# Performance work log

Measured on AMD Instinct MI355X. Metric: run time of the kernel, lower is better.

## Reference

```python
import jax, jax.numpy as jnp
from jax import lax
import numpy as np

B, S_SRC, S_TRG = 128, 128, 64
LEX_V, LEX_D = 32000, 300
NT_V, NT_D = 128, 128
H, CTX, ATT = 1024, 300, 100
DIN = LEX_D + 2 * NT_D + CTX  # decoder LSTM input: [ans_embed | context]


def setup_inputs():
    key = jax.random.key(0)
    ks = iter(jax.random.split(key, 40))
    g = lambda shape, s=0.05: jax.random.normal(next(ks), shape, dtype=jnp.float32) * s
    src_seqs = jax.random.randint(next(ks), (B, S_SRC), 1, LEX_V)
    src_lengths = jnp.sort(jax.random.randint(next(ks), (B,), 1, S_SRC + 1))[::-1]
    src_lengths = src_lengths.at[0].set(S_SRC)  # packed seqs sorted desc, max len = S_SRC
    trg_nt = jax.random.randint(next(ks), (B, S_TRG), 1, NT_V)
    par_nt = jax.random.randint(next(ks), (B, S_TRG), 1, NT_V)
    par_lex = jax.random.randint(next(ks), (B, S_TRG), 1, LEX_V)
    lex_emb = g((LEX_V, LEX_D), 1.0).at[0].set(0.0)  # padding_idx=0 zeroed
    nt_emb = g((NT_V, NT_D), 1.0).at[0].set(0.0)
    return {
        'src_seqs': src_seqs, 'src_lengths': src_lengths,
        'trg_nt': trg_nt, 'par_nt': par_nt, 'par_lex': par_lex,
        'lex_emb': lex_emb, 'nt_emb': nt_emb,
        'enc_Wih': g((4 * H, LEX_D)), 'enc_Whh': g((4 * H, H)), 'enc_b': g((4 * H,)),
        'dec_Wih': g((4 * H, DIN)), 'dec_Whh': g((4 * H, H)), 'dec_b': g((4 * H,)),
        'Wh1': g((2 * H, H)), 'bh1': g((2 * H,)), 'Wh2': g((H, 2 * H)), 'bh2': g((H,)),
        'Wc1': g((2 * H, H)), 'bc1': g((2 * H,)), 'Wc2': g((H, 2 * H)), 'bc2': g((H,)),
        'Wa': g((ATT, H)), 'ba': g((ATT,)),
        'Wqk': g((ATT, H)), 'bqk': g((ATT,)),
        'Wqv': g((CTX, H)), 'bqv': g((CTX,)),
    }


def lstm_cell(x, h, c, Wih, Whh, b):
    z = x @ Wih.T + h @ Whh.T + b
    i, f, g, o = jnp.split(z, 4, axis=-1)  # torch gate order i,f,g,o
    c2 = jax.nn.sigmoid(f) * c + jax.nn.sigmoid(i) * jnp.tanh(g)
    h2 = jax.nn.sigmoid(o) * jnp.tanh(c2)
    return h2, c2


def reference(src_seqs, src_lengths, trg_nt, par_nt, par_lex,
              lex_emb, nt_emb,
              enc_Wih, enc_Whh, enc_b, dec_Wih, dec_Whh, dec_b,
              Wh1, bh1, Wh2, bh2, Wc1, bc1, Wc2, bc2,
              Wa, ba, Wqk, bqk, Wqv, bqv):
    # ---- encoder LSTM over packed src (mask past lengths) ----
    src_embed = lex_emb[src_seqs]                       # (B,S,LEX_D)
    h0 = jnp.zeros((B, H), jnp.float32)

    def enc_step(carry, inp):
        h, c = carry
        xt, t = inp
        h2, c2 = lstm_cell(xt, h, c, enc_Wih, enc_Whh, enc_b)
        valid = (t < src_lengths)[:, None]
        h = jnp.where(valid, h2, h)
        c = jnp.where(valid, c2, c)
        return (h, c), jnp.where(valid, h2, 0.0)

    (hT, cT), outs = lax.scan(enc_step, (h0, h0),
                              (jnp.swapaxes(src_embed, 0, 1), jnp.arange(S_SRC)))
    src_hidden = jnp.swapaxes(outs, 0, 1)               # (B,S,H), zeros past length

    # ---- init decoder hidden via MLP transforms ----
    dh = jax.nn.relu(hT @ Wh1.T + bh1) @ Wh2.T + bh2
    dc = jax.nn.relu(cT @ Wc1.T + bc1) @ Wc2.T + bc2

    # ---- attention keys/values (src-side is step-invariant) ----
    q_key = jnp.tanh(src_hidden @ Wqk.T + bqk)          # (B,S,ATT)
    q_value = src_hidden @ Wqv.T + bqv                  # (B,S,CTX)
    mask = jnp.arange(S_SRC)[None, :] < src_lengths[:, None]

    ans_embed = jnp.concatenate(
        [nt_emb[trg_nt], nt_emb[par_nt], lex_emb[par_lex]], axis=2)  # (B,T,LEX_D+2*NT_D)

    def dec_step(carry, xt):
        h, c = carry
        a_key = jnp.tanh(h @ Wa.T + ba)                 # (B,ATT)
        energy = jnp.einsum('bsk,bk->bs', q_key, a_key)
        energy = jnp.where(mask, energy, -1e9)
        w = jax.nn.softmax(energy, axis=1)
        context = jnp.einsum('bs,bsd->bd', w, q_value)  # (B,CTX)
        inp = jnp.concatenate([xt, context], axis=1)    # (B,DIN)
        h2, c2 = lstm_cell(inp, h, c, dec_Wih, dec_Whh, dec_b)
        return (h2, c2), h2

    _, dec_outs = lax.scan(dec_step, (dh, dc), jnp.swapaxes(ans_embed, 0, 1))
    return jnp.swapaxes(dec_outs, 0, 1)                 # (B,T,H)
```

## Files before the change

kernel.cpp:

```cpp
#include <hip/hip_runtime.h>


constexpr int B_ = 128, S_ = 128, T_ = 64, H_ = 1024;
constexpr int KE_ = 1344;
constexpr int KD_ = 1920;
constexpr int KCE = KE_ / 32, KCD = KD_ / 32;

using bf16x8 = __attribute__((ext_vector_type(8))) __bf16;
using f32x4  = __attribute__((ext_vector_type(4))) float;
using ull = unsigned long long;

union Pack8 { ull q[2]; bf16x8 v; };

__device__ __forceinline__ float ldf(const void* p, size_t i, bool bf) {
  return bf ? (float)((const __bf16*)p)[i] : ((const float*)p)[i];
}
__device__ __forceinline__ float sigf(float x) { return 1.f / (1.f + __expf(-x)); }
__device__ __forceinline__ float tanf_(float x) { return 1.f - 2.f / (1.f + __expf(2.f * x)); }

__device__ __forceinline__ ull al8(const ull* p) {
  return __hip_atomic_load(p, __ATOMIC_RELAXED, __HIP_MEMORY_SCOPE_AGENT);
}
__device__ __forceinline__ void as8(ull* p, ull v) {
  __hip_atomic_store(p, v, __ATOMIC_RELAXED, __HIP_MEMORY_SCOPE_AGENT);
}

__device__ __forceinline__ void gbar(unsigned* bar, int bb, unsigned ep) {
  __syncthreads();
  if (threadIdx.x == 0)
    __hip_atomic_fetch_add(&bar[(bb & 15) * 32], 1u, __ATOMIC_RELAXED,
                           __HIP_MEMORY_SCOPE_AGENT);
  if (threadIdx.x < 16) {
    const unsigned tgt = ep * 16;
    while (__hip_atomic_load(&bar[threadIdx.x * 32], __ATOMIC_RELAXED,
                             __HIP_MEMORY_SCOPE_AGENT) < tgt)
      __builtin_amdgcn_s_sleep(2);
  }
  __syncthreads();
}

__global__ void sniff(const void* __restrict__ lex, int* __restrict__ flag) {
  if (threadIdx.x == 0 && blockIdx.x == 0) {
    const unsigned short* u = (const unsigned short*)lex;
    int garbage = 0;
    for (int i = 0; i < 64; ++i) {
      unsigned short v = u[1000000 + 2 * i];
      int ex = (v >> 7) & 0xFF;
      bool sane = ((v & 0x7FFF) == 0) || (ex >= 107 && ex <= 147);
      if (!sane) ++garbage;
    }
    *flag = (garbage >= 16) ? 0 : 1;
  }
}

__global__ void cvt_to_f32(const void* __restrict__ src, float* __restrict__ dst,
                           int n, const int* __restrict__ flag) {
  int i = blockIdx.x * blockDim.x + threadIdx.x;
  bool bf = *flag != 0;
  if (i < n) dst[i] = ldf(src, i, bf);
}

__global__ void f2b(const float* __restrict__ s, __bf16* __restrict__ d, int n) {
  int i = blockIdx.x * blockDim.x + threadIdx.x;
  if (i < n) d[i] = (__bf16)s[i];
}

__global__ void zero_state(__bf16* __restrict__ h, float* __restrict__ c) {
  int i = blockIdx.x * blockDim.x + threadIdx.x;
  if (i < B_ * H_) { h[i] = (__bf16)0.f; c[i] = 0.f; }
}

__global__ void zero_bar(unsigned* __restrict__ bar) {
  bar[threadIdx.x] = 0u;
}

__global__ void build_w_enc_sw(const void* __restrict__ Wih, const void* __restrict__ Whh,
                               __bf16* __restrict__ W, const int* __restrict__ flag) {
  int bid = blockIdx.x;
  int ug = bid >> 1, nt = bid & 1;
  bool bf = *flag != 0;
  for (int i = threadIdx.x; i < KCE * 512; i += blockDim.x) {
    int kc = i >> 9, rem = i & 511, lane = rem >> 3, j = rem & 7;
    int col = lane & 15, quad = lane >> 4;
    int gate = nt * 2 + (col >> 3), ul = col & 7;
    int r = gate * 1024 + ug * 8 + ul;
    int k = kc * 32 + quad * 8 + j;
    float v;
    if (k < 320) v = (k < 300) ? ldf(Wih, (size_t)r * 300 + k, bf) : 0.f;
    else         v = ldf(Whh, (size_t)r * 1024 + (k - 320), bf);
    W[(((size_t)bid * KCE + kc) * 64 + lane) * 8 + j] = (__bf16)v;
  }
}

__global__ void build_w_dec_sw(const void* __restrict__ Wih, const void* __restrict__ Whh,
                               __bf16* __restrict__ W, const int* __restrict__ flag) {
  int bid = blockIdx.x;
  int ug = bid >> 1, nt = bid & 1;
  bool bf = *flag != 0;
  for (int i = threadIdx.x; i < KCD * 512; i += blockDim.x) {
    int kc = i >> 9, rem = i & 511, lane = rem >> 3, j = rem & 7;
    int col = lane & 15, quad = lane >> 4;
    int gate = nt * 2 + (col >> 3), ul = col & 7;
    int r = gate * 1024 + ug * 8 + ul;
    int k = kc * 32 + quad * 8 + j;
    float v;
    if (k < 576)      v = (k < 556) ? ldf(Wih, (size_t)r * 856 + k, bf) : 0.f;
    else if (k < 896) { int kk = k - 576; v = (kk < 300) ? ldf(Wih, (size_t)r * 856 + 556 + kk, bf) : 0.f; }
    else              v = ldf(Whh, (size_t)r * 1024 + (k - 896), bf);
    W[(((size_t)bid * KCD + kc) * 64 + lane) * 8 + j] = (__bf16)v;
  }
}

__global__ void pad_cvt(const void* __restrict__ src, __bf16* __restrict__ dst,
                        int N, int K, int Kpad, const int* __restrict__ flag) {
  int n = blockIdx.x;
  bool bf = *flag != 0;
  for (int k = threadIdx.x; k < Kpad; k += blockDim.x) {
    float v = (n < N && k < K) ? ldf(src, (size_t)n * K + k, bf) : 0.f;
    dst[(size_t)n * Kpad + k] = (__bf16)v;
  }
}

__global__ void gather_emb(const void* __restrict__ lex, const int* __restrict__ seq,
                           __bf16* __restrict__ dst, const int* __restrict__ flag) {
  int blk = blockIdx.x;
  int t = blk >> 7, b = blk & 127;
  int id = seq[b * S_ + t];
  bool bf = *flag != 0;
  for (int k = threadIdx.x; k < 320; k += blockDim.x) {
    float v = (k < 300) ? ldf(lex, (size_t)id * 300 + k, bf) : 0.f;
    dst[(size_t)blk * 320 + k] = (__bf16)v;
  }
}

__global__ void gather_ans(const void* __restrict__ nt, const void* __restrict__ lex,
                           const int* __restrict__ trg, const int* __restrict__ par,
                           const int* __restrict__ plex, __bf16* __restrict__ dst,
                           const int* __restrict__ flag) {
  int blk = blockIdx.x;
  int t = blk >> 7, b = blk & 127;
  int i1 = trg[b * T_ + t], i2 = par[b * T_ + t], i3 = plex[b * T_ + t];
  bool bf = *flag != 0;
  for (int k = threadIdx.x; k < 576; k += blockDim.x) {
    float v = 0.f;
    if (k < 128)      v = ldf(nt, (size_t)i1 * 128 + k, bf);
    else if (k < 256) v = ldf(nt, (size_t)i2 * 128 + (k - 128), bf);
    else if (k < 556) v = ldf(lex, (size_t)i3 * 300 + (k - 256), bf);
    dst[(size_t)blk * 576 + k] = (__bf16)v;
  }
}

template <int ACT, bool WB, bool WF>
__global__ __launch_bounds__(256)
void gemm16(const __bf16* __restrict__ A, int lda,
            const __bf16* __restrict__ W, int K,
            const float* __restrict__ bias, int Nreal,
            __bf16* __restrict__ Cb, float* __restrict__ Cf, int ldc) {
  const int lane = threadIdx.x & 63;
  const int wave = threadIdx.x >> 6;
  const int col = lane & 15, quad = lane >> 4, koff = quad * 8;
  const int n0 = blockIdx.x * 16;
  const int m0 = blockIdx.y * 64 + wave * 16;
  f32x4 acc = {0.f, 0.f, 0.f, 0.f};
  const __bf16* ap = A + (size_t)(m0 + col) * lda + koff;
  const __bf16* wp = W + (size_t)(n0 + col) * K + koff;
  for (int k0 = 0; k0 < K; k0 += 32) {
    bf16x8 af = *(const bf16x8*)(ap + k0);
    bf16x8 bf = *(const bf16x8*)(wp + k0);
    acc = __builtin_amdgcn_mfma_f32_16x16x32_bf16(af, bf, acc, 0, 0, 0);
  }
  int n = n0 + col;
  float bv = (n < Nreal) ? bias[n] : 0.f;
#pragma unroll
  for (int r = 0; r < 4; ++r) {
    int m = m0 + quad * 4 + r;
    float v = acc[r] + bv;
    if (ACT == 1) v = fmaxf(v, 0.f);
    if (ACT == 2) v = tanf_(v);
    size_t idx = (size_t)m * ldc + n;
    if (WB) Cb[idx] = (__bf16)v;
    if (WF) Cf[idx] = v;
  }
}

__global__ void transpose_qk(const float* __restrict__ q, float* __restrict__ qT) {
  int b = blockIdx.x;
  for (int i = threadIdx.x; i < 100 * 128; i += blockDim.x) {
    int k = i >> 7, s = i & 127;
    qT[((size_t)b * 100 + k) * 128 + s] = q[((size_t)b * 128 + s) * 112 + k];
  }
}

struct EncArgs {
  const __bf16* wE; const float* bEncF; const __bf16* embE;
  __bf16* h0; __bf16* h1; float* cE; const int* lens; __bf16* SH; unsigned* bar;
};

__global__ __launch_bounds__(256, 1)
void enc_coop(EncArgs a) {
  extern __shared__ char smem[];
  __bf16* Wl = (__bf16*)smem;
  float* zb = (float*)(smem + 2 * KCE * 512 * 2);
  __bf16* hbuf = (__bf16*)(smem + 2 * KCE * 512 * 2 + 64 * 33 * 4);
  const int bb = blockIdx.x;
  const int ug = bb >> 1, mh = bb & 1;
  {
    const uint4* src = (const uint4*)(a.wE + (size_t)ug * 2 * KCE * 512);
    uint4* dst = (uint4*)Wl;
    for (int i = threadIdx.x; i < 2 * KCE * 512 * 2 / 16; i += 256) dst[i] = src[i];
  }
  const int tid = threadIdx.x;
  const int lane = tid & 63, wave = tid >> 6;
  const int col = lane & 15, quad = lane >> 4, koff = quad * 8;
  const int am = mh * 64 + wave * 16 + col;
  __syncthreads();

  for (int t = 0; t < S_; ++t) {
    const __bf16* hR = (t & 1) ? a.h1 : a.h0;
    __bf16* hW = (t & 1) ? a.h0 : a.h1;
    f32x4 acc0 = {0.f, 0.f, 0.f, 0.f}, acc1 = {0.f, 0.f, 0.f, 0.f};
    const __bf16* embRow = a.embE + ((size_t)t * B_ + am) * 320 + koff;
    const ull* hRow8 = (const ull*)(hR + (size_t)am * H_) + quad * 2;
#pragma unroll
    for (int kc = 0; kc < KCE; ++kc) {
      const int k0 = kc * 32;
      bf16x8 af;
      if (k0 < 320) {
        af = *(const bf16x8*)(embRow + k0);
      } else {
        Pack8 u2;
        u2.q[0] = al8(hRow8 + ((k0 - 320) >> 2));
        u2.q[1] = al8(hRow8 + ((k0 - 320) >> 2) + 1);
        af = u2.v;
      }
      bf16x8 b0 = *(const bf16x8*)(Wl + ((size_t)(0 * KCE + kc) * 64 + lane) * 8);
      bf16x8 b1 = *(const bf16x8*)(Wl + ((size_t)(1 * KCE + kc) * 64 + lane) * 8);
      acc0 = __builtin_amdgcn_mfma_f32_16x16x32_bf16(af, b0, acc0, 0, 0, 0);
      acc1 = __builtin_amdgcn_mfma_f32_16x16x32_bf16(af, b1, acc1, 0, 0, 0);
    }
#pragma unroll
    for (int r = 0; r < 4; ++r) {
      int ml = wave * 16 + quad * 4 + r;
      zb[ml * 33 + col] = acc0[r];
      zb[ml * 33 + 16 + col] = acc1[r];
    }
    __syncthreads();
#pragma unroll
    for (int p = 0; p < 2; ++p) {
      int idx = tid + p * 256;
      int ml = idx >> 3, u = idx & 7;
      int m = mh * 64 + ml, j = ug * 8 + u;
      float ig = sigf(zb[ml * 33 + u]       + a.bEncF[j]);
      float fg = sigf(zb[ml * 33 + 8 + u]   + a.bEncF[1024 + j]);
      float gg = tanf_(zb[ml * 33 + 16 + u] + a.bEncF[2048 + j]);
      float og = sigf(zb[ml * 33 + 24 + u]  + a.bEncF[3072 + j]);
      size_t sidx = (size_t)m * H_ + j;
      float cOld = a.cE[sidx];
      float c2 = fg * cOld + ig * gg;
      float h2 = og * tanf_(c2);
      bool valid = t < a.lens[m];
      a.cE[sidx] = valid ? c2 : cOld;
      hbuf[ml * 8 + u] = (__bf16)h2;
      a.SH[((size_t)m * S_ + t) * H_ + j] = valid ? (__bf16)h2 : (__bf16)0.f;
    }
    __syncthreads();
    if (tid < 128) {
      int ml = tid >> 1, u0 = (tid & 1) * 4;
      int m = mh * 64 + ml;
      ull nv = *(const ull*)(hbuf + ml * 8 + u0);
      if (t >= a.lens[m]) nv = al8((const ull*)(hR + (size_t)m * H_ + ug * 8 + u0));
      as8((ull*)(hW + (size_t)m * H_ + ug * 8 + u0), nv);
    }
    if (t != S_ - 1) gbar(a.bar, bb, t + 1);
  }
}

struct DecArgs {
  const __bf16* wD; const float* bDecF; const __bf16* ansP;
  __bf16* h0; __bf16* h1; float* cD; const int* lens;
  const __bf16* waB; const float* baF; const float* qkT; const float* qval;
  __bf16* ctx; void* out; const int* flag; unsigned* bar;
};

__global__ __launch_bounds__(256, 1)
void dec_coop(DecArgs a) {
  extern __shared__ char smem[];
  __bf16* Wl = (__bf16*)smem;
  float* zb = (float*)(smem + 2 * KCD * 512 * 2);
  __bf16* hbuf = (__bf16*)(smem + 2 * KCD * 512 * 2 + 64 * 33 * 4);
  const int bb = blockIdx.x;
  const int ug = bb >> 1, mh = bb & 1;
  {
    const uint4* src = (const uint4*)(a.wD + (size_t)ug * 2 * KCD * 512);
    uint4* dst = (uint4*)Wl;
    for (int i = threadIdx.x; i < 2 * KCD * 512 * 2 / 16; i += 256) dst[i] = src[i];
  }
  const int tid = threadIdx.x;
  const int lane = tid & 63, wave = tid >> 6;
  const int col = lane & 15, quad = lane >> 4, koff = quad * 8;
  const int am = mh * 64 + wave * 16 + col;
  const bool obf = *a.flag != 0;
  __syncthreads();

  for (int t = 0; t < T_; ++t) {
    const __bf16* hR = (t & 1) ? a.h1 : a.h0;
    __bf16* hW = (t & 1) ? a.h0 : a.h1;
    if (bb < B_) {
      const int b = bb;
      float* ak = zb; float* wts = zb + 112; float* sc = zb + 240; float* ctxb = zb + 368;
      const ull* hp = (const ull*)(hR + (size_t)b * H_);
      Pack8 u0, u1;
      u0.q[0] = al8(hp + lane * 4 + 0); u0.q[1] = al8(hp + lane * 4 + 1);
      u1.q[0] = al8(hp + lane * 4 + 2); u1.q[1] = al8(hp + lane * 4 + 3);
      float hf[16];
#pragma unroll
      for (int j2 = 0; j2 < 8; ++j2) { hf[j2] = (float)u0.v[j2]; hf[8 + j2] = (float)u1.v[j2]; }
      for (int n = wave; n < 100; n += 4) {
        bf16x8 w0 = *(const bf16x8*)(a.waB + (size_t)n * 1024 + lane * 16);
        bf16x8 w1 = *(const bf16x8*)(a.waB + (size_t)n * 1024 + lane * 16 + 8);
        float acc = 0.f;
#pragma unroll
        for (int j2 = 0; j2 < 8; ++j2)
          acc += hf[j2] * (float)w0[j2] + hf[8 + j2] * (float)w1[j2];
#pragma unroll
        for (int off = 32; off > 0; off >>= 1) acc += __shfl_xor(acc, off);
        if (lane == 0) ak[n] = tanf_(acc + a.baF[n]);
      }
      __syncthreads();
      int len = a.lens[b];
      if (tid < S_) {
        float e = -1e30f;
        if (tid < len) {
          float acc = 0.f;
#pragma unroll 4
          for (int k = 0; k < 100; ++k)
            acc += a.qkT[((size_t)b * 100 + k) * 128 + tid] * ak[k];
          e = acc;
        }
        wts[tid] = e; sc[tid] = e;
      }
      __syncthreads();
      for (int off = 64; off > 0; off >>= 1) {
        if (tid < off) sc[tid] = fmaxf(sc[tid], sc[tid + off]);
        __syncthreads();
      }
      float mx = sc[0];
      __syncthreads();
      if (tid < S_) {
        float ex = (wts[tid] <= -1e29f) ? 0.f : __expf(wts[tid] - mx);
        wts[tid] = ex; sc[tid] = ex;
      }
      __syncthreads();
      for (int off = 64; off > 0; off >>= 1) {
        if (tid < off) sc[tid] += sc[tid + off];
        __syncthreads();
      }
      float inv = 1.f / sc[0];
      for (int d = tid; d < 320; d += 256) {
        float v = 0.f;
        if (d < 300) {
#pragma unroll 8
          for (int s = 0; s < S_; ++s) v += wts[s] * a.qval[((size_t)b * S_ + s) * 304 + d];
          v *= inv;
        }
        ctxb[d] = v;
      }
      __syncthreads();
      if (tid < 80) {
        __bf16 p4[4];
#pragma unroll
        for (int i2 = 0; i2 < 4; ++i2) p4[i2] = (__bf16)ctxb[tid * 4 + i2];
        as8((ull*)a.ctx + (size_t)b * 80 + tid, *(const ull*)p4);
      }
    }
    gbar(a.bar, bb, 2 * t + 1);
    f32x4 acc0 = {0.f, 0.f, 0.f, 0.f}, acc1 = {0.f, 0.f, 0.f, 0.f};
    const __bf16* ansRow = a.ansP + ((size_t)t * B_ + am) * 576 + koff;
    const ull* ctxRow8 = (const ull*)a.ctx + (size_t)am * 80 + quad * 2;
    const ull* hRow8 = (const ull*)(hR + (size_t)am * H_) + quad * 2;
#pragma unroll
    for (int kc = 0; kc < KCD; ++kc) {
      const int k0 = kc * 32;
      bf16x8 af;
      if (k0 < 576) {
        af = *(const bf16x8*)(ansRow + k0);
      } else if (k0 < 896) {
        Pack8 u2;
        u2.q[0] = al8(ctxRow8 + ((k0 - 576) >> 2));
        u2.q[1] = al8(ctxRow8 + ((k0 - 576) >> 2) + 1);
        af = u2.v;
      } else {
        Pack8 u2;
        u2.q[0] = al8(hRow8 + ((k0 - 896) >> 2));
        u2.q[1] = al8(hRow8 + ((k0 - 896) >> 2) + 1);
        af = u2.v;
      }
      bf16x8 b0 = *(const bf16x8*)(Wl + ((size_t)(0 * KCD + kc) * 64 + lane) * 8);
      bf16x8 b1 = *(const bf16x8*)(Wl + ((size_t)(1 * KCD + kc) * 64 + lane) * 8);
      acc0 = __builtin_amdgcn_mfma_f32_16x16x32_bf16(af, b0, acc0, 0, 0, 0);
      acc1 = __builtin_amdgcn_mfma_f32_16x16x32_bf16(af, b1, acc1, 0, 0, 0);
    }
#pragma unroll
    for (int r = 0; r < 4; ++r) {
      int ml = wave * 16 + quad * 4 + r;
      zb[ml * 33 + col] = acc0[r];
      zb[ml * 33 + 16 + col] = acc1[r];
    }
    __syncthreads();
#pragma unroll
    for (int p = 0; p < 2; ++p) {
      int idx = tid + p * 256;
      int ml = idx >> 3, u = idx & 7;
      int m = mh * 64 + ml, j = ug * 8 + u;
      float ig = sigf(zb[ml * 33 + u]       + a.bDecF[j]);
      float fg = sigf(zb[ml * 33 + 8 + u]   + a.bDecF[1024 + j]);
      float gg = tanf_(zb[ml * 33 + 16 + u] + a.bDecF[2048 + j]);
      float og = sigf(zb[ml * 33 + 24 + u]  + a.bDecF[3072 + j]);
      size_t sidx = (size_t)m * H_ + j;
      float cOld = a.cD[sidx];
      float c2 = fg * cOld + ig * gg;
      float h2 = og * tanf_(c2);
      a.cD[sidx] = c2;
      hbuf[ml * 8 + u] = (__bf16)h2;
      size_t oidx = ((size_t)m * T_ + t) * H_ + j;
      if (obf) ((__bf16*)a.out)[oidx] = (__bf16)h2;
      else     ((float*)a.out)[oidx] = h2;
    }
    __syncthreads();
    if (tid < 128) {
      int ml = tid >> 1, u0 = (tid & 1) * 4;
      int m = mh * 64 + ml;
      ull nv = *(const ull*)(hbuf + ml * 8 + u0);
      as8((ull*)(hW + (size_t)m * H_ + ug * 8 + u0), nv);
    }
    if (t != T_ - 1) gbar(a.bar, bb, 2 * t + 2);
  }
}

extern "C" void kernel_launch(void* const* d_in, const int* in_sizes, int n_in,
                              void* d_out, int out_size, void* d_ws, size_t ws_size,
                              hipStream_t stream) {
  const int* src_seqs = (const int*)d_in[0];
  const int* src_len  = (const int*)d_in[1];
  const int* trg_nt   = (const int*)d_in[2];
  const int* par_nt   = (const int*)d_in[3];
  const int* par_lex  = (const int*)d_in[4];
  const void* lex_emb = d_in[5];
  const void* nt_emb  = d_in[6];
  const void* encWih  = d_in[7];
  const void* encWhh  = d_in[8];
  const void* encB    = d_in[9];
  const void* decWih  = d_in[10];
  const void* decWhh  = d_in[11];
  const void* decB    = d_in[12];
  const void* Wh1 = d_in[13]; const void* bh1 = d_in[14];
  const void* Wh2 = d_in[15]; const void* bh2 = d_in[16];
  const void* Wc1 = d_in[17]; const void* bc1 = d_in[18];
  const void* Wc2 = d_in[19]; const void* bc2 = d_in[20];
  const void* Wa  = d_in[21]; const void* ba  = d_in[22];
  const void* Wqk = d_in[23]; const void* bqk = d_in[24];
  const void* Wqv = d_in[25]; const void* bqv = d_in[26];

  char* base = (char*)d_ws;
  size_t off = 0;
  auto alloc = [&](size_t bytes) -> char* {
    char* p = base + off;
    off += (bytes + 255) & ~(size_t)255;
    return p;
  };
  __bf16* wEnc = (__bf16*)alloc((size_t)4096 * KE_ * 2);
  float*  bEncF = (float*)alloc(4096 * 4);
  __bf16* wDec = (__bf16*)alloc((size_t)4096 * KD_ * 2);
  float*  bDecF = (float*)alloc(4096 * 4);
  __bf16* embE = (__bf16*)alloc((size_t)S_ * B_ * 320 * 2);
  __bf16* ansP = (__bf16*)alloc((size_t)T_ * B_ * 576 * 2);
  __bf16* SH   = (__bf16*)alloc((size_t)B_ * S_ * H_ * 2);
  __bf16* wh1p = (__bf16*)alloc((size_t)2048 * 1024 * 2);
  __bf16* wh2p = (__bf16*)alloc((size_t)1024 * 2048 * 2);
  __bf16* wc1p = (__bf16*)alloc((size_t)2048 * 1024 * 2);
  __bf16* wc2p = (__bf16*)alloc((size_t)1024 * 2048 * 2);
  __bf16* wqkp = (__bf16*)alloc((size_t)112 * 1024 * 2);
  __bf16* wqvp = (__bf16*)alloc((size_t)304 * 1024 * 2);
  __bf16* waB  = (__bf16*)alloc((size_t)112 * 1024 * 2);
  float*  qkey = (float*)alloc((size_t)B_ * S_ * 112 * 4);
  float*  qkT  = (float*)alloc((size_t)B_ * 100 * 128 * 4);
  float*  qval = (float*)alloc((size_t)B_ * S_ * 304 * 4);
  __bf16* hE0 = (__bf16*)alloc((size_t)B_ * H_ * 2);
  __bf16* hE1 = (__bf16*)alloc((size_t)B_ * H_ * 2);
  float*  cE  = (float*)alloc((size_t)B_ * H_ * 4);
  __bf16* cEb = (__bf16*)alloc((size_t)B_ * H_ * 2);
  __bf16* t1b = (__bf16*)alloc((size_t)B_ * 2048 * 2);
  __bf16* t2b = (__bf16*)alloc((size_t)B_ * 2048 * 2);
  __bf16* hD0 = (__bf16*)alloc((size_t)B_ * H_ * 2);
  __bf16* hD1 = (__bf16*)alloc((size_t)B_ * H_ * 2);
  float*  cD  = (float*)alloc((size_t)B_ * H_ * 4);
  __bf16* ctx = (__bf16*)alloc((size_t)B_ * 320 * 2);
  float*  bh1F = (float*)alloc(2048 * 4);
  float*  bh2F = (float*)alloc(1024 * 4);
  float*  bc1F = (float*)alloc(2048 * 4);
  float*  bc2F = (float*)alloc(1024 * 4);
  float*  baF  = (float*)alloc(112 * 4);
  float*  bqkF = (float*)alloc(112 * 4);
  float*  bqvF = (float*)alloc(304 * 4);
  unsigned* bar = (unsigned*)alloc(1024 * 4);
  int*    flag = (int*)alloc(256);
  if (off > ws_size) return;

  sniff<<<1, 64, 0, stream>>>(lex_emb, flag);
  zero_bar<<<1, 1024, 0, stream>>>(bar);
  cvt_to_f32<<<16, 256, 0, stream>>>(encB, bEncF, 4096, flag);
  cvt_to_f32<<<16, 256, 0, stream>>>(decB, bDecF, 4096, flag);
  cvt_to_f32<<<8, 256, 0, stream>>>(bh1, bh1F, 2048, flag);
  cvt_to_f32<<<4, 256, 0, stream>>>(bh2, bh2F, 1024, flag);
  cvt_to_f32<<<8, 256, 0, stream>>>(bc1, bc1F, 2048, flag);
  cvt_to_f32<<<4, 256, 0, stream>>>(bc2, bc2F, 1024, flag);
  cvt_to_f32<<<1, 256, 0, stream>>>(ba, baF, 100, flag);
  cvt_to_f32<<<1, 256, 0, stream>>>(bqk, bqkF, 100, flag);
  cvt_to_f32<<<2, 256, 0, stream>>>(bqv, bqvF, 300, flag);
  build_w_enc_sw<<<256, 512, 0, stream>>>(encWih, encWhh, wEnc, flag);
  build_w_dec_sw<<<256, 512, 0, stream>>>(decWih, decWhh, wDec, flag);
  pad_cvt<<<2048, 256, 0, stream>>>(Wh1, wh1p, 2048, 1024, 1024, flag);
  pad_cvt<<<1024, 256, 0, stream>>>(Wh2, wh2p, 1024, 2048, 2048, flag);
  pad_cvt<<<2048, 256, 0, stream>>>(Wc1, wc1p, 2048, 1024, 1024, flag);
  pad_cvt<<<1024, 256, 0, stream>>>(Wc2, wc2p, 1024, 2048, 2048, flag);
  pad_cvt<<<112, 256, 0, stream>>>(Wqk, wqkp, 100, 1024, 1024, flag);
  pad_cvt<<<304, 256, 0, stream>>>(Wqv, wqvp, 300, 1024, 1024, flag);
  pad_cvt<<<100, 256, 0, stream>>>(Wa, waB, 100, 1024, 1024, flag);
  gather_emb<<<S_ * B_, 256, 0, stream>>>(lex_emb, src_seqs, embE, flag);
  gather_ans<<<T_ * B_, 256, 0, stream>>>(nt_emb, lex_emb, trg_nt, par_nt, par_lex, ansP, flag);
  zero_state<<<512, 256, 0, stream>>>(hE0, cE);

  const unsigned encLds = 2 * KCE * 512 * 2 + 64 * 33 * 4 + 1024;
  const unsigned decLds = 2 * KCD * 512 * 2 + 64 * 33 * 4 + 1024;
  hipFuncSetAttribute((const void*)enc_coop, hipFuncAttributeMaxDynamicSharedMemorySize, encLds);
  hipFuncSetAttribute((const void*)dec_coop, hipFuncAttributeMaxDynamicSharedMemorySize, decLds);

  EncArgs ea = {wEnc, bEncF, embE, hE0, hE1, cE, src_len, SH, bar};
  void* eargs[] = {&ea};
  hipLaunchCooperativeKernel((const void*)enc_coop, dim3(256), dim3(256), eargs, encLds, stream);

  f2b<<<512, 256, 0, stream>>>(cE, cEb, B_ * H_);
  gemm16<1, true, false><<<dim3(128, 2), 256, 0, stream>>>(hE0, 1024, wh1p, 1024, bh1F, 2048, t1b, nullptr, 2048);
  gemm16<0, true, false><<<dim3(64, 2), 256, 0, stream>>>(t1b, 2048, wh2p, 2048, bh2F, 1024, hD0, nullptr, 1024);
  gemm16<1, true, false><<<dim3(128, 2), 256, 0, stream>>>(cEb, 1024, wc1p, 1024, bc1F, 2048, t2b, nullptr, 2048);
  gemm16<0, false, true><<<dim3(64, 2), 256, 0, stream>>>(t2b, 2048, wc2p, 2048, bc2F, 1024, nullptr, cD, 1024);

  gemm16<2, false, true><<<dim3(7, 256), 256, 0, stream>>>(SH, 1024, wqkp, 1024, bqkF, 100, nullptr, qkey, 112);
  transpose_qk<<<B_, 256, 0, stream>>>(qkey, qkT);
  gemm16<0, false, true><<<dim3(19, 256), 256, 0, stream>>>(SH, 1024, wqvp, 1024, bqvF, 300, nullptr, qval, 304);

  DecArgs da = {wDec, bDecF, ansP, hD0, hD1, cD, src_len,
                waB, baF, qkT, qval, ctx, d_out, flag, bar + 512};
  void* dargs[] = {&da};
  hipLaunchCooperativeKernel((const void*)dec_coop, dim3(256), dim3(256), dargs, decLds, stream);
}
```

Measured before the change: 5.676 ms.

## Split grid barriers and overlap input projections with recurrent waits

Splits the grid barrier into separate arrive and wait phases. The next step's input-side matmul (embeddings or answer embeddings) is computed between arrive and wait, so it overlaps the barrier latency. In the decoder, the per-step attention barrier is replaced by per-row context flags: each block runs its hidden-state MFMAs first and only waits for the rows it needs. Attention softmax now uses wavefront shuffle reductions, q_key and q_value are written pre-transposed by the GEMM epilogue, and SH is stored time-major with vectorized writes. This adds extra flag traffic and subtler memory-ordering assumptions in exchange for shorter serialized critical paths.

After: 4.762 ms. 16.1% less time.

```diff
diff --git a/kernel.cpp b/kernel.cpp
--- a/kernel.cpp
+++ b/kernel.cpp
@@ -11,6 +11,7 @@
 using ull = unsigned long long;
 
 union Pack8 { ull q[2]; bf16x8 v; };
+union Pack4 { __bf16 h[4]; ull q; };
 
 __device__ __forceinline__ float ldf(const void* p, size_t i, bool bf) {
   return bf ? (float)((const __bf16*)p)[i] : ((const float*)p)[i];
@@ -24,17 +25,21 @@
 __device__ __forceinline__ void as8(ull* p, ull v) {
   __hip_atomic_store(p, v, __ATOMIC_RELAXED, __HIP_MEMORY_SCOPE_AGENT);
 }
-
-__device__ __forceinline__ void gbar(unsigned* bar, int bb, unsigned ep) {
-  __syncthreads();
+__device__ __forceinline__ unsigned alu(const unsigned* p) {
+  return __hip_atomic_load(p, __ATOMIC_RELAXED, __HIP_MEMORY_SCOPE_AGENT);
+}
+__device__ __forceinline__ void asu(unsigned* p, unsigned v) {
+  __hip_atomic_store(p, v, __ATOMIC_RELAXED, __HIP_MEMORY_SCOPE_AGENT);
+}
+
+__device__ __forceinline__ void garrive(unsigned* slots, int bb) {
   if (threadIdx.x == 0)
-    __hip_atomic_fetch_add(&bar[(bb & 15) * 32], 1u, __ATOMIC_RELAXED,
+    __hip_atomic_fetch_add(&slots[(bb & 31) * 32], 1u, __ATOMIC_RELAXED,
                            __HIP_MEMORY_SCOPE_AGENT);
-  if (threadIdx.x < 16) {
-    const unsigned tgt = ep * 16;
-    while (__hip_atomic_load(&bar[threadIdx.x * 32], __ATOMIC_RELAXED,
-                             __HIP_MEMORY_SCOPE_AGENT) < tgt)
-      __builtin_amdgcn_s_sleep(2);
+}
+__device__ __forceinline__ void gwait(unsigned* slots, unsigned tgt) {
+  if (threadIdx.x < 32) {
+    while (alu(&slots[threadIdx.x * 32]) < tgt) __builtin_amdgcn_s_sleep(1);
   }
   __syncthreads();
 }
@@ -71,7 +76,8 @@
 }
 
 __global__ void zero_bar(unsigned* __restrict__ bar) {
-  bar[threadIdx.x] = 0u;
+  int i = blockIdx.x * blockDim.x + threadIdx.x;
+  if (i < 2304) bar[i] = 0u;
 }
 
 __global__ void build_w_enc_sw(const void* __restrict__ Wih, const void* __restrict__ Whh,
@@ -150,7 +156,7 @@
   }
 }
 
-template <int ACT, bool WB, bool WF>
+template <int ACT, bool WB, bool WF, int OM>
 __global__ __launch_bounds__(256)
 void gemm16(const __bf16* __restrict__ A, int lda,
             const __bf16* __restrict__ W, int K,
@@ -177,17 +183,11 @@
     float v = acc[r] + bv;
     if (ACT == 1) v = fmaxf(v, 0.f);
     if (ACT == 2) v = tanf_(v);
-    size_t idx = (size_t)m * ldc + n;
+    size_t idx;
+    if (OM == 0) idx = (size_t)m * ldc + n;
+    else         idx = ((size_t)(m & 127) * ldc + n) * 128 + (m >> 7);
     if (WB) Cb[idx] = (__bf16)v;
     if (WF) Cf[idx] = v;
-  }
-}
-
-__global__ void transpose_qk(const float* __restrict__ q, float* __restrict__ qT) {
-  int b = blockIdx.x;
-  for (int i = threadIdx.x; i < 100 * 128; i += blockDim.x) {
-    int k = i >> 7, s = i & 127;
-    qT[((size_t)b * 100 + k) * 128 + s] = q[((size_t)b * 128 + s) * 112 + k];
   }
 }
 
@@ -213,31 +213,44 @@
   const int lane = tid & 63, wave = tid >> 6;
   const int col = lane & 15, quad = lane >> 4, koff = quad * 8;
   const int am = mh * 64 + wave * 16 + col;
+  const int e_u = tid & 7;
+  const int jj = ug * 8 + e_u;
+  const float bi = a.bEncF[jj], bff = a.bEncF[1024 + jj];
+  const float bg = a.bEncF[2048 + jj], bo = a.bEncF[3072 + jj];
+  const int m0p = mh * 64 + (tid >> 3);
+  const int len0 = a.lens[m0p], len1 = a.lens[m0p + 32];
+  const int pm = mh * 64 + (tid >> 1);
+  const int slen = (tid < 64) ? a.lens[mh * 64 + tid] : 0;
+  ull lastpub = 0;
   __syncthreads();
 
-  for (int t = 0; t < S_; ++t) {
-    const __bf16* hR = (t & 1) ? a.h1 : a.h0;
-    __bf16* hW = (t & 1) ? a.h0 : a.h1;
-    f32x4 acc0 = {0.f, 0.f, 0.f, 0.f}, acc1 = {0.f, 0.f, 0.f, 0.f};
-    const __bf16* embRow = a.embE + ((size_t)t * B_ + am) * 320 + koff;
-    const ull* hRow8 = (const ull*)(hR + (size_t)am * H_) + quad * 2;
-#pragma unroll
-    for (int kc = 0; kc < KCE; ++kc) {
-      const int k0 = kc * 32;
-      bf16x8 af;
-      if (k0 < 320) {
-        af = *(const bf16x8*)(embRow + k0);
-      } else {
-        Pack8 u2;
-        u2.q[0] = al8(hRow8 + ((k0 - 320) >> 2));
-        u2.q[1] = al8(hRow8 + ((k0 - 320) >> 2) + 1);
-        af = u2.v;
-      }
+  f32x4 acc0 = {0.f, 0.f, 0.f, 0.f}, acc1 = {0.f, 0.f, 0.f, 0.f};
+  {
+    const __bf16* eRow = a.embE + (size_t)am * 320 + koff;
+#pragma unroll
+    for (int kc = 0; kc < 10; ++kc) {
+      bf16x8 af = *(const bf16x8*)(eRow + kc * 32);
       bf16x8 b0 = *(const bf16x8*)(Wl + ((size_t)(0 * KCE + kc) * 64 + lane) * 8);
       bf16x8 b1 = *(const bf16x8*)(Wl + ((size_t)(1 * KCE + kc) * 64 + lane) * 8);
       acc0 = __builtin_amdgcn_mfma_f32_16x16x32_bf16(af, b0, acc0, 0, 0, 0);
       acc1 = __builtin_amdgcn_mfma_f32_16x16x32_bf16(af, b1, acc1, 0, 0, 0);
     }
+  }
+
+  for (int t = 0; t < S_; ++t) {
+    const __bf16* hR = (t & 1) ? a.h1 : a.h0;
+    __bf16* hW = (t & 1) ? a.h0 : a.h1;
+    const ull* hRow8 = (const ull*)(hR + (size_t)am * H_) + quad * 2;
+#pragma unroll
+    for (int kc = 10; kc < KCE; ++kc) {
+      Pack8 u2;
+      u2.q[0] = al8(hRow8 + (kc * 8 - 80));
+      u2.q[1] = al8(hRow8 + (kc * 8 - 80) + 1);
+      bf16x8 b0 = *(const bf16x8*)(Wl + ((size_t)(0 * KCE + kc) * 64 + lane) * 8);
+      bf16x8 b1 = *(const bf16x8*)(Wl + ((size_t)(1 * KCE + kc) * 64 + lane) * 8);
+      acc0 = __builtin_amdgcn_mfma_f32_16x16x32_bf16(u2.v, b0, acc0, 0, 0, 0);
+      acc1 = __builtin_amdgcn_mfma_f32_16x16x32_bf16(u2.v, b1, acc1, 0, 0, 0);
+    }
 #pragma unroll
     for (int r = 0; r < 4; ++r) {
       int ml = wave * 16 + quad * 4 + r;
@@ -247,39 +260,57 @@
     __syncthreads();
 #pragma unroll
     for (int p = 0; p < 2; ++p) {
-      int idx = tid + p * 256;
-      int ml = idx >> 3, u = idx & 7;
-      int m = mh * 64 + ml, j = ug * 8 + u;
-      float ig = sigf(zb[ml * 33 + u]       + a.bEncF[j]);
-      float fg = sigf(zb[ml * 33 + 8 + u]   + a.bEncF[1024 + j]);
-      float gg = tanf_(zb[ml * 33 + 16 + u] + a.bEncF[2048 + j]);
-      float og = sigf(zb[ml * 33 + 24 + u]  + a.bEncF[3072 + j]);
-      size_t sidx = (size_t)m * H_ + j;
+      int ml = (tid >> 3) + p * 32;
+      int m = mh * 64 + ml;
+      int len = p ? len1 : len0;
+      float ig = sigf(zb[ml * 33 + e_u] + bi);
+      float fg = sigf(zb[ml * 33 + 8 + e_u] + bff);
+      float gg = tanf_(zb[ml * 33 + 16 + e_u] + bg);
+      float og = sigf(zb[ml * 33 + 24 + e_u] + bo);
+      size_t sidx = (size_t)m * H_ + jj;
       float cOld = a.cE[sidx];
       float c2 = fg * cOld + ig * gg;
       float h2 = og * tanf_(c2);
-      bool valid = t < a.lens[m];
+      bool valid = t < len;
       a.cE[sidx] = valid ? c2 : cOld;
-      hbuf[ml * 8 + u] = (__bf16)h2;
-      a.SH[((size_t)m * S_ + t) * H_ + j] = valid ? (__bf16)h2 : (__bf16)0.f;
+      hbuf[ml * 8 + e_u] = (__bf16)h2;
     }
     __syncthreads();
     if (tid < 128) {
-      int ml = tid >> 1, u0 = (tid & 1) * 4;
-      int m = mh * 64 + ml;
-      ull nv = *(const ull*)(hbuf + ml * 8 + u0);
-      if (t >= a.lens[m]) nv = al8((const ull*)(hR + (size_t)m * H_ + ug * 8 + u0));
-      as8((ull*)(hW + (size_t)m * H_ + ug * 8 + u0), nv);
-    }
-    if (t != S_ - 1) gbar(a.bar, bb, t + 1);
+      ull nv = (t < ((tid & 1) ? a.lens[pm] : a.lens[pm])) ? ((const ull*)hbuf)[tid] : lastpub;
+      lastpub = nv;
+      as8((ull*)(hW + (size_t)pm * H_ + ug * 8) + (tid & 1), nv);
+    }
+    __syncthreads();
+    garrive(a.bar, bb);
+    if (tid < 64) {
+      int m = mh * 64 + tid;
+      uint4 val;
+      if (t < slen) val = *(const uint4*)(hbuf + tid * 8);
+      else { val.x = 0; val.y = 0; val.z = 0; val.w = 0; }
+      *(uint4*)(a.SH + ((size_t)t * B_ + m) * H_ + ug * 8) = val;
+    }
+    if (t != S_ - 1) {
+      acc0 = f32x4{0.f, 0.f, 0.f, 0.f}; acc1 = acc0;
+      const __bf16* eRow = a.embE + ((size_t)(t + 1) * B_ + am) * 320 + koff;
+#pragma unroll
+      for (int kc = 0; kc < 10; ++kc) {
+        bf16x8 af = *(const bf16x8*)(eRow + kc * 32);
+        bf16x8 b0 = *(const bf16x8*)(Wl + ((size_t)(0 * KCE + kc) * 64 + lane) * 8);
+        bf16x8 b1 = *(const bf16x8*)(Wl + ((size_t)(1 * KCE + kc) * 64 + lane) * 8);
+        acc0 = __builtin_amdgcn_mfma_f32_16x16x32_bf16(af, b0, acc0, 0, 0, 0);
+        acc1 = __builtin_amdgcn_mfma_f32_16x16x32_bf16(af, b1, acc1, 0, 0, 0);
+      }
+      gwait(a.bar, 8u * (unsigned)(t + 1));
+    }
   }
 }
 
 struct DecArgs {
   const __bf16* wD; const float* bDecF; const __bf16* ansP;
   __bf16* h0; __bf16* h1; float* cD; const int* lens;
-  const __bf16* waB; const float* baF; const float* qkT; const float* qval;
-  __bf16* ctx; void* out; const int* flag; unsigned* bar;
+  const __bf16* waB; const float* baF; const float* qkT; const float* qvT;
+  __bf16* ctx; void* out; const int* flag; unsigned* bar; unsigned* ctxFlag;
 };
 
 __global__ __launch_bounds__(256, 1)
@@ -299,15 +330,38 @@
   const int lane = tid & 63, wave = tid >> 6;
   const int col = lane & 15, quad = lane >> 4, koff = quad * 8;
   const int am = mh * 64 + wave * 16 + col;
+  const int m0w = mh * 64 + wave * 16;
   const bool obf = *a.flag != 0;
+  const int e_u = tid & 7;
+  const int jj = ug * 8 + e_u;
+  const float bi = a.bDecF[jj], bff = a.bDecF[1024 + jj];
+  const float bg = a.bDecF[2048 + jj], bo = a.bDecF[3072 + jj];
+  const int pm = mh * 64 + (tid >> 1);
+  const int alen = (bb < B_) ? a.lens[bb] : 0;
   __syncthreads();
+
+  f32x4 acc0 = {0.f, 0.f, 0.f, 0.f}, acc1 = {0.f, 0.f, 0.f, 0.f};
+  {
+    const __bf16* aRow = a.ansP + (size_t)am * 576 + koff;
+#pragma unroll
+    for (int kc = 0; kc < 18; ++kc) {
+      bf16x8 af = *(const bf16x8*)(aRow + kc * 32);
+      bf16x8 b0 = *(const bf16x8*)(Wl + ((size_t)(0 * KCD + kc) * 64 + lane) * 8);
+      bf16x8 b1 = *(const bf16x8*)(Wl + ((size_t)(1 * KCD + kc) * 64 + lane) * 8);
+      acc0 = __builtin_amdgcn_mfma_f32_16x16x32_bf16(af, b0, acc0, 0, 0, 0);
+      acc1 = __builtin_amdgcn_mfma_f32_16x16x32_bf16(af, b1, acc1, 0, 0, 0);
+    }
+  }
 
   for (int t = 0; t < T_; ++t) {
     const __bf16* hR = (t & 1) ? a.h1 : a.h0;
     __bf16* hW = (t & 1) ? a.h0 : a.h1;
     if (bb < B_) {
       const int b = bb;
-      float* ak = zb; float* wts = zb + 112; float* sc = zb + 240; float* ctxb = zb + 368;
+      float* ak = zb;
+      float* wts = zb + 112;
+      float* red = zb + 240;
+      float* ctxb = zb + 256;
       const ull* hp = (const ull*)(hR + (size_t)b * H_);
       Pack8 u0, u1;
       u0.q[0] = al8(hp + lane * 4 + 0); u0.q[1] = al8(hp + lane * 4 + 1);
@@ -327,79 +381,76 @@
         if (lane == 0) ak[n] = tanf_(acc + a.baF[n]);
       }
       __syncthreads();
-      int len = a.lens[b];
-      if (tid < S_) {
-        float e = -1e30f;
-        if (tid < len) {
-          float acc = 0.f;
+      float e = -3.0e38f;
+      if (tid < S_ && tid < alen) {
+        float acc = 0.f;
 #pragma unroll 4
-          for (int k = 0; k < 100; ++k)
-            acc += a.qkT[((size_t)b * 100 + k) * 128 + tid] * ak[k];
-          e = acc;
-        }
-        wts[tid] = e; sc[tid] = e;
+        for (int k = 0; k < 100; ++k)
+          acc += a.qkT[((size_t)b * 112 + k) * 128 + tid] * ak[k];
+        e = acc;
       }
+      float r = e;
+#pragma unroll
+      for (int off = 32; off > 0; off >>= 1) r = fmaxf(r, __shfl_xor(r, off));
+      if (tid == 0) red[0] = r;
+      if (tid == 64) red[1] = r;
       __syncthreads();
-      for (int off = 64; off > 0; off >>= 1) {
-        if (tid < off) sc[tid] = fmaxf(sc[tid], sc[tid + off]);
-        __syncthreads();
-      }
-      float mx = sc[0];
+      float mx = fmaxf(red[0], red[1]);
+      float ex = (tid < S_ && tid < alen) ? __expf(e - mx) : 0.f;
+      if (tid < S_) wts[tid] = ex;
+      float sm = ex;
+#pragma unroll
+      for (int off = 32; off > 0; off >>= 1) sm += __shfl_xor(sm, off);
+      if (tid == 0) red[2] = sm;
+      if (tid == 64) red[3] = sm;
       __syncthreads();
-      if (tid < S_) {
-        float ex = (wts[tid] <= -1e29f) ? 0.f : __expf(wts[tid] - mx);
-        wts[tid] = ex; sc[tid] = ex;
-      }
-      __syncthreads();
-      for (int off = 64; off > 0; off >>= 1) {
-        if (tid < off) sc[tid] += sc[tid + off];
-        __syncthreads();
-      }
-      float inv = 1.f / sc[0];
+      float inv = 1.f / (red[2] + red[3]);
       for (int d = tid; d < 320; d += 256) {
         float v = 0.f;
         if (d < 300) {
+          const float* qp = a.qvT + ((size_t)b * 304 + d) * 128;
 #pragma unroll 8
-          for (int s = 0; s < S_; ++s) v += wts[s] * a.qval[((size_t)b * S_ + s) * 304 + d];
+          for (int s2 = 0; s2 < S_; ++s2) v += wts[s2] * qp[s2];
           v *= inv;
         }
         ctxb[d] = v;
       }
       __syncthreads();
       if (tid < 80) {
-        __bf16 p4[4];
-#pragma unroll
-        for (int i2 = 0; i2 < 4; ++i2) p4[i2] = (__bf16)ctxb[tid * 4 + i2];
-        as8((ull*)a.ctx + (size_t)b * 80 + tid, *(const ull*)p4);
+        Pack4 pk;
+#pragma unroll
+        for (int i2 = 0; i2 < 4; ++i2) pk.h[i2] = (__bf16)ctxb[tid * 4 + i2];
+        as8((ull*)a.ctx + (size_t)b * 80 + tid, pk.q);
       }
-    }
-    gbar(a.bar, bb, 2 * t + 1);
-    f32x4 acc0 = {0.f, 0.f, 0.f, 0.f}, acc1 = {0.f, 0.f, 0.f, 0.f};
-    const __bf16* ansRow = a.ansP + ((size_t)t * B_ + am) * 576 + koff;
-    const ull* ctxRow8 = (const ull*)a.ctx + (size_t)am * 80 + quad * 2;
+      __syncthreads();
+      if (tid == 0) asu(&a.ctxFlag[b], (unsigned)(t + 1));
+    }
     const ull* hRow8 = (const ull*)(hR + (size_t)am * H_) + quad * 2;
 #pragma unroll
-    for (int kc = 0; kc < KCD; ++kc) {
-      const int k0 = kc * 32;
-      bf16x8 af;
-      if (k0 < 576) {
-        af = *(const bf16x8*)(ansRow + k0);
-      } else if (k0 < 896) {
-        Pack8 u2;
-        u2.q[0] = al8(ctxRow8 + ((k0 - 576) >> 2));
-        u2.q[1] = al8(ctxRow8 + ((k0 - 576) >> 2) + 1);
-        af = u2.v;
-      } else {
-        Pack8 u2;
-        u2.q[0] = al8(hRow8 + ((k0 - 896) >> 2));
-        u2.q[1] = al8(hRow8 + ((k0 - 896) >> 2) + 1);
-        af = u2.v;
-      }
+    for (int kc = 28; kc < KCD; ++kc) {
+      Pack8 u2;
+      u2.q[0] = al8(hRow8 + (kc * 8 - 224));
+      u2.q[1] = al8(hRow8 + (kc * 8 - 224) + 1);
       bf16x8 b0 = *(const bf16x8*)(Wl + ((size_t)(0 * KCD + kc) * 64 + lane) * 8);
       bf16x8 b1 = *(const bf16x8*)(Wl + ((size_t)(1 * KCD + kc) * 64 + lane) * 8);
-      acc0 = __builtin_amdgcn_mfma_f32_16x16x32_bf16(af, b0, acc0, 0, 0, 0);
-      acc1 = __builtin_amdgcn_mfma_f32_16x16x32_bf16(af, b1, acc1, 0, 0, 0);
-    }
+      acc0 = __builtin_amdgcn_mfma_f32_16x16x32_bf16(u2.v, b0, acc0, 0, 0, 0);
+      acc1 = __builtin_amdgcn_mfma_f32_16x16x32_bf16(u2.v, b1, acc1, 0, 0, 0);
+    }
+    if (lane < 16) {
+      while (alu(&a.ctxFlag[m0w + lane]) < (unsigned)(t + 1)) __builtin_amdgcn_s_sleep(1);
+    }
+    const ull* ctxRow8 = (const ull*)a.ctx + (size_t)am * 80 + quad * 2;
+#pragma unroll
+    for (int kc = 18; kc < 28; ++kc) {
+      Pack8 u2;
+      u2.q[0] = al8(ctxRow8 + (kc * 8 - 144));
+      u2.q[1] = al8(ctxRow8 + (kc * 8 - 144) + 1);
+      bf16x8 b0 = *(const bf16x8*)(Wl + ((size_t)(0 * KCD + kc) * 64 + lane) * 8);
+      bf16x8 b1 = *(const bf16x8*)(Wl + ((size_t)(1 * KCD + kc) * 64 + lane) * 8);
+      acc0 = __builtin_amdgcn_mfma_f32_16x16x32_bf16(u2.v, b0, acc0, 0, 0, 0);
+      acc1 = __builtin_amdgcn_mfma_f32_16x16x32_bf16(u2.v, b1, acc1, 0, 0, 0);
+    }
+    __syncthreads();
 #pragma unroll
     for (int r = 0; r < 4; ++r) {
       int ml = wave * 16 + quad * 4 + r;
@@ -409,31 +460,44 @@
     __syncthreads();
 #pragma unroll
     for (int p = 0; p < 2; ++p) {
-      int idx = tid + p * 256;
-      int ml = idx >> 3, u = idx & 7;
-      int m = mh * 64 + ml, j = ug * 8 + u;
-      float ig = sigf(zb[ml * 33 + u]       + a.bDecF[j]);
-      float fg = sigf(zb[ml * 33 + 8 + u]   + a.bDecF[1024 + j]);
-      float gg = tanf_(zb[ml * 33 + 16 + u] + a.bDecF[2048 + j]);
-      float og = sigf(zb[ml * 33 + 24 + u]  + a.bDecF[3072 + j]);
-      size_t sidx = (size_t)m * H_ + j;
+      int ml = (tid >> 3) + p * 32;
+      int m = mh * 64 + ml;
+      float ig = sigf(zb[ml * 33 + e_u] + bi);
+      float fg = sigf(zb[ml * 33 + 8 + e_u] + bff);
+      float gg = tanf_(zb[ml * 33 + 16 + e_u] + bg);
+      float og = sigf(zb[ml * 33 + 24 + e_u] + bo);
+      size_t sidx = (size_t)m * H_ + jj;
       float cOld = a.cD[sidx];
       float c2 = fg * cOld + ig * gg;
       float h2 = og * tanf_(c2);
       a.cD[sidx] = c2;
-      hbuf[ml * 8 + u] = (__bf16)h2;
-      size_t oidx = ((size_t)m * T_ + t) * H_ + j;
-      if (obf) ((__bf16*)a.out)[oidx] = (__bf16)h2;
-      else     ((float*)a.out)[oidx] = h2;
+      hbuf[ml * 8 + e_u] = (__bf16)h2;
+      if (!obf) ((float*)a.out)[((size_t)m * T_ + t) * H_ + jj] = h2;
     }
     __syncthreads();
     if (tid < 128) {
-      int ml = tid >> 1, u0 = (tid & 1) * 4;
-      int m = mh * 64 + ml;
-      ull nv = *(const ull*)(hbuf + ml * 8 + u0);
-      as8((ull*)(hW + (size_t)m * H_ + ug * 8 + u0), nv);
-    }
-    if (t != T_ - 1) gbar(a.bar, bb, 2 * t + 2);
+      as8((ull*)(hW + (size_t)pm * H_ + ug * 8) + (tid & 1), ((const ull*)hbuf)[tid]);
+    }
+    __syncthreads();
+    garrive(a.bar, bb);
+    if (obf && tid < 64) {
+      int m = mh * 64 + tid;
+      *(uint4*)((__bf16*)a.out + ((size_t)m * T_ + t) * H_ + ug * 8) =
+          *(const uint4*)(hbuf + tid * 8);
+    }
+    if (t != T_ - 1) {
+      acc0 = f32x4{0.f, 0.f, 0.f, 0.f}; acc1 = acc0;
+      const __bf16* aRow = a.ansP + ((size_t)(t + 1) * B_ + am) * 576 + koff;
+#pragma unroll
+      for (int kc = 0; kc < 18; ++kc) {
+        bf16x8 af = *(const bf16x8*)(aRow + kc * 32);
+        bf16x8 b0 = *(const bf16x8*)(Wl + ((size_t)(0 * KCD + kc) * 64 + lane) * 8);
+        bf16x8 b1 = *(const bf16x8*)(Wl + ((size_t)(1 * KCD + kc) * 64 + lane) * 8);
+        acc0 = __builtin_amdgcn_mfma_f32_16x16x32_bf16(af, b0, acc0, 0, 0, 0);
+        acc1 = __builtin_amdgcn_mfma_f32_16x16x32_bf16(af, b1, acc1, 0, 0, 0);
+      }
+      gwait(a.bar, 8u * (unsigned)(t + 1));
+    }
   }
 }
 
@@ -482,9 +546,8 @@
   __bf16* wqkp = (__bf16*)alloc((size_t)112 * 1024 * 2);
   __bf16* wqvp = (__bf16*)alloc((size_t)304 * 1024 * 2);
   __bf16* waB  = (__bf16*)alloc((size_t)112 * 1024 * 2);
-  float*  qkey = (float*)alloc((size_t)B_ * S_ * 112 * 4);
-  float*  qkT  = (float*)alloc((size_t)B_ * 100 * 128 * 4);
-  float*  qval = (float*)alloc((size_t)B_ * S_ * 304 * 4);
+  float*  qkT  = (float*)alloc((size_t)B_ * 112 * 128 * 4);
+  float*  qvT  = (float*)alloc((size_t)B_ * 304 * 128 * 4);
   __bf16* hE0 = (__bf16*)alloc((size_t)B_ * H_ * 2);
   __bf16* hE1 = (__bf16*)alloc((size_t)B_ * H_ * 2);
   float*  cE  = (float*)alloc((size_t)B_ * H_ * 4);
@@ -502,12 +565,12 @@
   float*  baF  = (float*)alloc(112 * 4);
   float*  bqkF = (float*)alloc(112 * 4);
   float*  bqvF = (float*)alloc(304 * 4);
-  unsigned* bar = (unsigned*)alloc(1024 * 4);
+  unsigned* bar = (unsigned*)alloc(2304 * 4);
   int*    flag = (int*)alloc(256);
   if (off > ws_size) return;
 
   sniff<<<1, 64, 0, stream>>>(lex_emb, flag);
-  zero_bar<<<1, 1024, 0, stream>>>(bar);
+  zero_bar<<<3, 1024, 0, stream>>>(bar);
   cvt_to_f32<<<16, 256, 0, stream>>>(encB, bEncF, 4096, flag);
   cvt_to_f32<<<16, 256, 0, stream>>>(decB, bDecF, 4096, flag);
   cvt_to_f32<<<8, 256, 0, stream>>>(bh1, bh1F, 2048, flag);
@@ -540,17 +603,16 @@
   hipLaunchCooperativeKernel((const void*)enc_coop, dim3(256), dim3(256), eargs, encLds, stream);
 
   f2b<<<512, 256, 0, stream>>>(cE, cEb, B_ * H_);
-  gemm16<1, true, false><<<dim3(128, 2), 256, 0, stream>>>(hE0, 1024, wh1p, 1024, bh1F, 2048, t1b, nullptr, 2048);
-  gemm16<0, true, false><<<dim3(64, 2), 256, 0, stream>>>(t1b, 2048, wh2p, 2048, bh2F, 1024, hD0, nullptr, 1024);
-  gemm16<1, true, false><<<dim3(128, 2), 256, 0, stream>>>(cEb, 1024, wc1p, 1024, bc1F, 2048, t2b, nullptr, 2048);
-  gemm16<0, false, true><<<dim3(64, 2), 256, 0, stream>>>(t2b, 2048, wc2p, 2048, bc2F, 1024, nullptr, cD, 1024);
-
-  gemm16<2, false, true><<<dim3(7, 256), 256, 0, stream>>>(SH, 1024, wqkp, 1024, bqkF, 100, nullptr, qkey, 112);
-  transpose_qk<<<B_, 256, 0, stream>>>(qkey, qkT);
-  gemm16<0, false, true><<<dim3(19, 256), 256, 0, stream>>>(SH, 1024, wqvp, 1024, bqvF, 300, nullptr, qval, 304);
+  gemm16<1, true, false, 0><<<dim3(128, 2), 256, 0, stream>>>(hE0, 1024, wh1p, 1024, bh1F, 2048, t1b, nullptr, 2048);
+  gemm16<0, true, false, 0><<<dim3(64, 2), 256, 0, stream>>>(t1b, 2048, wh2p, 2048, bh2F, 1024, hD0, nullptr, 1024);
+  gemm16<1, true, false, 0><<<dim3(128, 2), 256, 0, stream>>>(cEb, 1024, wc1p, 1024, bc1F, 2048, t2b, nullptr, 2048);
+  gemm16<0, false, true, 0><<<dim3(64, 2), 256, 0, stream>>>(t2b, 2048, wc2p, 2048, bc2F, 1024, nullptr, cD, 1024);
+
+  gemm16<2, false, true, 1><<<dim3(7, 256), 256, 0, stream>>>(SH, 1024, wqkp, 1024, bqkF, 100, nullptr, qkT, 112);
+  gemm16<0, false, true, 1><<<dim3(19, 256), 256, 0, stream>>>(SH, 1024, wqvp, 1024, bqvF, 300, nullptr, qvT, 304);
 
   DecArgs da = {wDec, bDecF, ansP, hD0, hD1, cD, src_len,
-                waB, baF, qkT, qval, ctx, d_out, flag, bar + 512};
+                waB, baF, qkT, qvT, ctx, d_out, flag, bar + 1024, bar + 2048};
   void* dargs[] = {&da};
   hipLaunchCooperativeKernel((const void*)dec_coop, dim3(256), dim3(256), dargs, decLds, stream);
 }
```
